# Kernel tuning notes

Hardware: AMD Instinct MI355X
Metric: run time of the kernel (lower is better)

The kernel has to match this reference:

```python
import jax, jax.numpy as jnp
import numpy as np

THRESHOLD = 0.5
ALPHA = 1.0
RATIO = 1.0
BACKGROUND = 0
OBJECT = 1


def cxcywh_to_xyxy(b):
    cxcy, wh = b[..., :2], b[..., 2:]
    return jnp.concatenate([cxcy - wh / 2.0, cxcy + wh / 2.0], axis=-1)


def xyxy_to_cxcywh(b):
    xy1, xy2 = b[..., :2], b[..., 2:]
    return jnp.concatenate([(xy1 + xy2) / 2.0, xy2 - xy1], axis=-1)


def cxcywh_to_gcxgcy(c, d):
    # standard SSD encoding with variances (0.1, 0.2)
    g_cxcy = (c[..., :2] - d[..., :2]) / (d[..., 2:] / 10.0)
    g_wh = jnp.log(c[..., 2:] / d[..., 2:]) * 5.0
    return jnp.concatenate([g_cxcy, g_wh], axis=-1)


def box_iou(a, b):
    # a: [M,4] xyxy, b: [A,4] xyxy -> [M,A]
    area_a = (a[:, 2] - a[:, 0]) * (a[:, 3] - a[:, 1])
    area_b = (b[:, 2] - b[:, 0]) * (b[:, 3] - b[:, 1])
    lt = jnp.maximum(a[:, None, :2], b[None, :, :2])
    rb = jnp.minimum(a[:, None, 2:], b[None, :, 2:])
    wh = jnp.clip(rb - lt, 0.0)
    inter = wh[..., 0] * wh[..., 1]
    return inter / (area_a[:, None] + area_b[None, :] - inter)


def setup_inputs() -> dict:
    B, A, M = 32, 16384, 64
    key = jax.random.key(0)
    k1, k2, k3, k4 = jax.random.split(key, 4)
    x = jax.random.normal(k1, (B, A, 4), dtype=jnp.float32)
    y = jax.random.normal(k2, (B, A, 2), dtype=jnp.float32)
    # valid xyxy GT boxes in [0,1]
    u = jax.random.uniform(k3, (B, M, 4), dtype=jnp.float32)
    xy1 = u[..., :2] * 0.7
    wh = 0.05 + u[..., 2:] * 0.25
    boxes = jnp.concatenate([xy1, xy1 + wh], axis=-1)
    # default (prior) boxes in cxcywh
    ud = jax.random.uniform(k4, (A, 4), dtype=jnp.float32)
    dcxcy = 0.05 + ud[..., :2] * 0.9
    dwh = 0.05 + ud[..., 2:] * 0.25
    default = jnp.concatenate([dcxcy, dwh], axis=-1)
    labels = jnp.ones((B, M), dtype=jnp.int32)  # all GT boxes are 'object'
    return {"x": x, "y": y, "boxes": boxes, "labels": labels, "default": default}


def reference(x, y, boxes, labels, default):
    B, A = x.shape[0], default.shape[0]
    M = boxes.shape[1]
    default_xy = cxcywh_to_xyxy(default)  # [A,4]

    def match(bx):  # bx: [M,4]
        iou = box_iou(bx, default_xy)              # [M,A]
        overlap = iou.max(axis=0)                  # [A] best GT per anchor
        digit = jnp.argmax(iou, axis=0)            # [A]
        best_anchor = jnp.argmax(iou, axis=1)      # [M] best anchor per GT
        digit = digit.at[best_anchor].set(jnp.arange(M))
        overlap = overlap.at[best_anchor].set(1.0)
        return digit, overlap

    digit, overlap = jax.vmap(match)(boxes)        # [B,A], [B,A]
    matched = jnp.take_along_axis(boxes, digit[..., None], axis=1)  # [B,A,4]
    localization = cxcywh_to_gcxgcy(xyxy_to_cxcywh(matched), default)  # [B,A,4]

    gathered = jnp.take_along_axis(labels, digit, axis=1)           # [B,A]
    classification = jnp.where(overlap < THRESHOLD, BACKGROUND, gathered)

    positives = classification == OBJECT
    total = positives.sum()
    totf = total.astype(x.dtype)

    # SmoothL1 (beta=1), mean over positive elements (P*4)
    d = x - localization
    ad = jnp.abs(d)
    sl1 = jnp.where(ad < 1.0, 0.5 * d * d, ad - 0.5)
    smooth = (sl1 * positives[..., None]).sum() / (totf * 4.0)

    # per-anchor cross entropy
    logp = jax.nn.log_softmax(y, axis=-1)                 # [B,A,2]
    ent = -jnp.take_along_axis(logp, classification[..., None], axis=-1)[..., 0]

    pos_sum = jnp.where(positives, ent, 0.0).sum()
    # hard negative mining: sort negatives descending, keep int(total*ratio)
    negv = jnp.where(positives, 0.0, ent).ravel()         # CE >= 0, so masking with 0 is safe
    neg_sorted = jnp.sort(negv)[::-1]
    keep = (totf * RATIO).astype(jnp.int32)
    neg_sum = jnp.where(jnp.arange(negv.shape[0]) < keep, neg_sorted, 0.0).sum()

    entropy = ALPHA * (pos_sum + neg_sum) / totf
    return smooth + entropy
```

## Files before the change

### kernel.cpp

```cpp
#include <hip/hip_runtime.h>

#define THRESH 0.5f

__global__ void __launch_bounds__(256) k_matchboth(
        const float* __restrict__ boxes, const float* __restrict__ dflt,
        unsigned* __restrict__ match, unsigned long long* __restrict__ bestchunk,
        unsigned* __restrict__ zerop, int B, int A, int M, int chunks) {
    __shared__ float4 bx[128];
    __shared__ float barea[128];
    __shared__ float4 anch[256];
    __shared__ float adarea[256];
    __shared__ unsigned long long lm[128];
    int tid = threadIdx.x;
    if (blockIdx.x == 0) {
        for (int j = tid; j < 6160; j += 256) zerop[j] = 0u;
    }
    int b = blockIdx.x / chunks;
    int chunk = blockIdx.x - b * chunks;
    int a = chunk * 256 + tid;
    if (tid < M) {
        float4 bv = *reinterpret_cast<const float4*>(boxes + ((size_t)b * M + tid) * 4);
        bx[tid] = bv;
        barea[tid] = (bv.z - bv.x) * (bv.w - bv.y);
        lm[tid] = 0ull;
    }
    bool aval = (a < A);
    float dx1 = 0.f, dy1 = 0.f, dx2 = 0.f, dy2 = 0.f, darea = 0.f;
    if (aval) {
        float4 dv = *reinterpret_cast<const float4*>(dflt + (size_t)a * 4);
        dx1 = dv.x - dv.z * 0.5f; dy1 = dv.y - dv.w * 0.5f;
        dx2 = dv.x + dv.z * 0.5f; dy2 = dv.y + dv.w * 0.5f;
        darea = (dx2 - dx1) * (dy2 - dy1);
    }
    anch[tid] = make_float4(dx1, dy1, dx2, dy2);
    adarea[tid] = darea;
    __syncthreads();
    if (aval) {
        float binter = -1.0f, bS = 1.0f; int bm = 0;
        #pragma unroll 4
        for (int m = 0; m < M; ++m) {
            float4 bb = bx[m];
            float lx = fmaxf(bb.x, dx1), ly = fmaxf(bb.y, dy1);
            float rx = fminf(bb.z, dx2), ry = fminf(bb.w, dy2);
            float w = fmaxf(rx - lx, 0.f), h = fmaxf(ry - ly, 0.f);
            float inter = w * h;
            float S = barea[m] + darea;
            bool gt = inter * bS > binter * S;
            binter = gt ? inter : binter;
            bS     = gt ? S : bS;
            bm     = gt ? m : bm;
        }
        unsigned fl = (3.0f * binter >= bS) ? (1u << 30) : 0u;
        match[(size_t)b * A + a] = (unsigned)bm | fl;
    }
    int wv = tid >> 6, lane = tid & 63;
    int abase = chunk * 256 + wv * 64;
    int kmax = min(64, A - abase);
    if (lane < M && kmax > 0) {
        float4 bb = bx[lane];
        float ba = barea[lane];
        float binter = -1.0f, bS = 1.0f; int bk = 0;
        #pragma unroll 4
        for (int k = 0; k < kmax; ++k) {
            float4 av = anch[wv * 64 + k];
            float lx = fmaxf(bb.x, av.x), ly = fmaxf(bb.y, av.y);
            float rx = fminf(bb.z, av.z), ry = fminf(bb.w, av.w);
            float w = fmaxf(rx - lx, 0.f), h = fmaxf(ry - ly, 0.f);
            float inter = w * h;
            float S = ba + adarea[wv * 64 + k];
            bool gt = inter * bS > binter * S;
            binter = gt ? inter : binter;
            bS     = gt ? S : bS;
            bk     = gt ? k : bk;
        }
        float best = binter / (bS - binter);
        atomicMax(&lm[lane], ((unsigned long long)__float_as_uint(best) << 32) |
                             (unsigned long long)(unsigned)(~(abase + bk)));
    }
    __syncthreads();
    if (tid < M)
        bestchunk[((size_t)b * chunks + chunk) * M + tid] = lm[tid];
}

__global__ void k_override(const unsigned long long* __restrict__ bestchunk,
                           unsigned* __restrict__ match, int B, int A, int M, int chunks) {
    int i = blockIdx.x * blockDim.x + threadIdx.x;
    if (i >= B * M) return;
    int b = i / M, m = i - b * M;
    const unsigned long long* bp = bestchunk + (size_t)b * chunks * M + m;
    unsigned long long p = 0ull;
    for (int c = 0; c < chunks; ++c) {
        unsigned long long q = bp[(size_t)c * M];
        p = (q > p) ? q : p;
    }
    unsigned a = ~(unsigned)(p & 0xFFFFFFFFull);
    if (a < (unsigned)A)
        atomicMax(&match[(size_t)b * A + a], 0x80000000u | (unsigned)m);
}

__global__ void __launch_bounds__(256) k_main(
        const float* __restrict__ x, const float* __restrict__ y,
        const float* __restrict__ boxes, const int* __restrict__ labels,
        const float* __restrict__ dflt, const unsigned* __restrict__ match,
        float* __restrict__ negv, unsigned* __restrict__ hist1,
        unsigned* __restrict__ scal, int A, int M, int N) {
    __shared__ unsigned lh[2048];
    __shared__ float4 sbx[128];
    __shared__ int slab[128];
    int tid = threadIdx.x;
    int i0 = (blockIdx.x * 256 + tid) * 4;
    int b = (int)(((long long)blockIdx.x * 1024) / A);
    uint4 w4 = *reinterpret_cast<const uint4*>(match + i0);
    const float4* yp = reinterpret_cast<const float4*>(y + (size_t)i0 * 2);
    float4 ya = yp[0], yb = yp[1];
    for (int j = tid; j < 2048; j += 256) lh[j] = 0u;
    if (tid < M) {
        sbx[tid] = *reinterpret_cast<const float4*>(boxes + ((size_t)b * M + tid) * 4);
        slab[tid] = labels[b * M + tid];
    }
    __syncthreads();
    float l_smooth = 0.f, l_pos = 0.f; int l_cnt = 0;
    {
        unsigned wws[4] = {w4.x, w4.y, w4.z, w4.w};
        float y0s[4] = {ya.x, ya.z, yb.x, yb.z};
        float y1s[4] = {ya.y, ya.w, yb.y, yb.w};
        float vs[4];
        int a0 = i0 - b * A;
        #pragma unroll
        for (int e = 0; e < 4; ++e) {
            unsigned w = wws[e];
            int digit = (int)(w & 0xFFFFu);
            bool flag = (w & 0xC0000000u) != 0u;
            int c = flag ? slab[digit] : 0;
            bool pos = (c == 1);
            float y0 = y0s[e], y1v = y1s[e];
            float mx = fmaxf(y0, y1v);
            float lse = mx + log1pf(expf(-fabsf(y0 - y1v)));
            float ent = lse - ((c == 0) ? y0 : y1v);
            float v = pos ? 0.f : ent;
            vs[e] = v;
            if (pos) {
                float4 bv = sbx[digit];
                float4 dv = *reinterpret_cast<const float4*>(dflt + (size_t)(a0 + e) * 4);
                float4 xv = *reinterpret_cast<const float4*>(x + (size_t)(i0 + e) * 4);
                float cw = bv.z - bv.x, ch = bv.w - bv.y;
                float ccx = (bv.x + bv.z) * 0.5f, ccy = (bv.y + bv.w) * 0.5f;
                float l0 = (ccx - dv.x) / (dv.z * 0.1f);
                float l1 = (ccy - dv.y) / (dv.w * 0.1f);
                float l2 = logf(cw / dv.z) * 5.f;
                float l3 = logf(ch / dv.w) * 5.f;
                float s = 0.f, d, ad;
                d = xv.x - l0; ad = fabsf(d); s += (ad < 1.f) ? 0.5f * d * d : ad - 0.5f;
                d = xv.y - l1; ad = fabsf(d); s += (ad < 1.f) ? 0.5f * d * d : ad - 0.5f;
                d = xv.z - l2; ad = fabsf(d); s += (ad < 1.f) ? 0.5f * d * d : ad - 0.5f;
                d = xv.w - l3; ad = fabsf(d); s += (ad < 1.f) ? 0.5f * d * d : ad - 0.5f;
                l_smooth += s; l_pos += ent; l_cnt += 1;
            }
            atomicAdd(&lh[__float_as_uint(v) >> 21], 1u);
        }
        *reinterpret_cast<float4*>(negv + i0) = make_float4(vs[0], vs[1], vs[2], vs[3]);
    }
    for (int off = 32; off > 0; off >>= 1) {
        l_smooth += __shfl_down(l_smooth, off, 64);
        l_pos    += __shfl_down(l_pos, off, 64);
        l_cnt    += __shfl_down(l_cnt, off, 64);
    }
    __shared__ float rs[4], rp[4]; __shared__ int rc[4];
    int wv = tid >> 6;
    if ((tid & 63) == 0) { rs[wv] = l_smooth; rp[wv] = l_pos; rc[wv] = l_cnt; }
    __syncthreads();
    if (tid == 0) {
        float ss = rs[0] + rs[1] + rs[2] + rs[3];
        float pp = rp[0] + rp[1] + rp[2] + rp[3];
        int   cc = rc[0] + rc[1] + rc[2] + rc[3];
        if (ss != 0.f) atomicAdd((float*)&scal[2], ss);
        if (pp != 0.f) atomicAdd((float*)&scal[1], pp);
        if (cc)        atomicAdd((int*)&scal[0], cc);
    }
    __syncthreads();
    for (int j = tid; j < 2048; j += 256) {
        unsigned h = lh[j];
        if (h) atomicAdd(&hist1[j], h);
    }
}

__device__ __forceinline__ void scan_find(const unsigned* hist, int nbins,
                                          unsigned k, unsigned* ts, unsigned* res) {
    int t = threadIdx.x;
    int per = nbins >> 8;
    unsigned s = 0;
    for (int j = 0; j < per; ++j) s += hist[t * per + j];
    ts[t] = s;
    __syncthreads();
    for (int off = 1; off < 256; off <<= 1) {
        unsigned add = (t >= off) ? ts[t - off] : 0u;
        __syncthreads();
        ts[t] += add;
        __syncthreads();
    }
    unsigned total = ts[255];
    unsigned P = (t == 0) ? 0u : ts[t - 1];
    for (int j = 0; j < per; ++j) {
        unsigned h = hist[t * per + j];
        P += h;
        unsigned above = total - P;
        if (above < k && k <= above + h) { res[0] = (unsigned)(t * per + j); res[1] = k - above; }
    }
    __syncthreads();
}

__global__ void __launch_bounds__(256) k_refine2(
        const float* __restrict__ negv, int N, unsigned* __restrict__ scal,
        const unsigned* __restrict__ hist1, unsigned* __restrict__ hist2,
        float* __restrict__ fsum2, float* __restrict__ out) {
    __shared__ unsigned ts[256], res[2];
    __shared__ unsigned lh[2048];
    __shared__ float lf[2048];
    int tid = threadIdx.x;
    scan_find(hist1, 2048, scal[0], ts, res);
    unsigned bin1 = res[0], k1 = res[1];
    for (int j = tid; j < 2048; j += 256) { lh[j] = 0u; lf[j] = 0.f; }
    __syncthreads();
    float sacc = 0.f;
    int i = (blockIdx.x * 256 + tid) * 4;
    if (i + 3 < N) {
        float4 v4 = *reinterpret_cast<const float4*>(negv + i);
        float vv[4] = {v4.x, v4.y, v4.z, v4.w};
        #pragma unroll
        for (int e = 0; e < 4; ++e) {
            unsigned u = __float_as_uint(vv[e]);
            unsigned b1 = u >> 21;
            if (b1 > bin1) sacc += vv[e];
            else if (b1 == bin1) {
                unsigned j = (u >> 10) & 0x7FFu;
                atomicAdd(&lh[j], 1u);
                atomicAdd(&lf[j], vv[e]);
            }
        }
    }
    __syncthreads();
    for (int j = tid; j < 2048; j += 256) {
        unsigned h = lh[j];
        if (h) { atomicAdd(&hist2[j], h); atomicAdd(&fsum2[j], lf[j]); }
    }
    for (int off = 32; off > 0; off >>= 1) sacc += __shfl_down(sacc, off, 64);
    __shared__ float rsum[4];
    __shared__ unsigned isLast;
    int wv = tid >> 6;
    if ((tid & 63) == 0) rsum[wv] = sacc;
    __syncthreads();
    if (tid == 0) {
        float ss = rsum[0] + rsum[1] + rsum[2] + rsum[3];
        if (ss != 0.f) atomicAdd((float*)&scal[9], ss);
        __threadfence();
        unsigned prev = atomicAdd(&scal[12], 1u);
        isLast = (prev == gridDim.x - 1) ? 1u : 0u;
    }
    __syncthreads();
    if (!isLast) return;
    for (int j = tid; j < 2048; j += 256) {
        lh[j] = ((volatile unsigned*)hist2)[j];
        lf[j] = ((volatile float*)fsum2)[j];
    }
    __syncthreads();
    scan_find(lh, 2048, k1, ts, res);
    unsigned bin2 = res[0], k2 = res[1];
    float fs = 0.f;
    for (int j = tid; j < 2048; j += 256)
        if (j > (int)bin2) fs += lf[j];
    for (int off = 32; off > 0; off >>= 1) fs += __shfl_down(fs, off, 64);
    if ((tid & 63) == 0) rsum[wv] = fs;
    __syncthreads();
    if (tid == 0) {
        float fst = rsum[0] + rsum[1] + rsum[2] + rsum[3];
        volatile unsigned* vs = scal;
        volatile float* vf = (volatile float*)scal;
        float k = (float)vs[0];
        float tmid = __uint_as_float((bin1 << 21) | (bin2 << 10) | 512u);
        float neg_sum = vf[9] + fst + (float)k2 * tmid;
        float smooth = vf[2] / (k * 4.f);
        float ent = (vf[1] + neg_sum) / k;
        out[0] = smooth + ent;
    }
}

extern "C" void kernel_launch(void* const* d_in, const int* in_sizes, int n_in,
                              void* d_out, int out_size, void* d_ws, size_t ws_size,
                              hipStream_t stream) {
    const float* x      = (const float*)d_in[0];
    const float* y      = (const float*)d_in[1];
    const float* boxes  = (const float*)d_in[2];
    const int*   labels = (const int*)d_in[3];
    const float* dflt   = (const float*)d_in[4];
    float* out = (float*)d_out;

    int A = in_sizes[4] / 4;
    int B = in_sizes[1] / (2 * A);
    int M = in_sizes[3] / B;
    int N = B * A;
    int chunks = (A + 255) / 256;

    unsigned* ws    = (unsigned*)d_ws;
    unsigned* match = ws;
    float*    negv  = (float*)(ws + (size_t)N);
    unsigned long long* bestchunk = (unsigned long long*)(ws + (size_t)2 * N);
    unsigned* hist1 = ws + (size_t)2 * N + (size_t)2 * B * chunks * M;
    unsigned* hist2 = hist1 + 2048;
    float*    fsum2 = (float*)(hist2 + 2048);
    unsigned* scal  = (unsigned*)(fsum2 + 2048);

    k_matchboth<<<dim3(B * chunks), dim3(256), 0, stream>>>(boxes, dflt, match, bestchunk,
                                                            hist1, B, A, M, chunks);
    k_override<<<dim3((B * M + 255) / 256), dim3(256), 0, stream>>>(bestchunk, match, B, A, M, chunks);
    k_main<<<dim3(N / 1024), dim3(256), 0, stream>>>(x, y, boxes, labels, dflt, match,
                                                     negv, hist1, scal, A, M, N);
    k_refine2<<<dim3(N / 1024), dim3(256), 0, stream>>>(negv, N, scal, hist1, hist2, fsum2, out);
}
```

Measured before the change: 161.7 us.

## Reduce per-box best anchor with global atomics and load x/default unconditionally

The per-chunk best-anchor array and the loop over chunks in k_override are replaced by a 64-bit atomicMax into one slot per (batch, box). A separate zeroing kernel now clears that slot array and the histogram and scalar buffers. In k_main, the x and default-box rows are loaded as contiguous vector loads up front and the SmoothL1 terms are computed for every anchor, which avoids divergent scattered loads at the cost of extra log/divide work. An extra kernel launch is added and the N bounds check in k_refine2 is dropped.

```diff
diff --git a/kernel.cpp b/kernel.cpp
--- a/kernel.cpp
+++ b/kernel.cpp
@@ -1,20 +1,22 @@
 #include <hip/hip_runtime.h>
 
 #define THRESH 0.5f
+
+__global__ void k_zero(unsigned* __restrict__ p, int n) {
+    int i = blockIdx.x * blockDim.x + threadIdx.x;
+    if (i < n) p[i] = 0u;
+}
 
 __global__ void __launch_bounds__(256) k_matchboth(
         const float* __restrict__ boxes, const float* __restrict__ dflt,
-        unsigned* __restrict__ match, unsigned long long* __restrict__ bestchunk,
-        unsigned* __restrict__ zerop, int B, int A, int M, int chunks) {
+        unsigned* __restrict__ match, unsigned long long* __restrict__ bestbox,
+        int B, int A, int M, int chunks) {
     __shared__ float4 bx[128];
     __shared__ float barea[128];
     __shared__ float4 anch[256];
     __shared__ float adarea[256];
     __shared__ unsigned long long lm[128];
     int tid = threadIdx.x;
-    if (blockIdx.x == 0) {
-        for (int j = tid; j < 6160; j += 256) zerop[j] = 0u;
-    }
     int b = blockIdx.x / chunks;
     int chunk = blockIdx.x - b * chunks;
     int a = chunk * 256 + tid;
@@ -78,24 +80,22 @@
                              (unsigned long long)(unsigned)(~(abase + bk)));
     }
     __syncthreads();
-    if (tid < M)
-        bestchunk[((size_t)b * chunks + chunk) * M + tid] = lm[tid];
-}
-
-__global__ void k_override(const unsigned long long* __restrict__ bestchunk,
-                           unsigned* __restrict__ match, int B, int A, int M, int chunks) {
+    if (tid < M) {
+        unsigned long long p = lm[tid];
+        if (p) atomicMax(&bestbox[(size_t)b * M + tid], p);
+    }
+}
+
+__global__ void k_override(const unsigned long long* __restrict__ bestbox,
+                           unsigned* __restrict__ match, int B, int A, int M) {
     int i = blockIdx.x * blockDim.x + threadIdx.x;
     if (i >= B * M) return;
-    int b = i / M, m = i - b * M;
-    const unsigned long long* bp = bestchunk + (size_t)b * chunks * M + m;
-    unsigned long long p = 0ull;
-    for (int c = 0; c < chunks; ++c) {
-        unsigned long long q = bp[(size_t)c * M];
-        p = (q > p) ? q : p;
-    }
+    unsigned long long p = bestbox[i];
     unsigned a = ~(unsigned)(p & 0xFFFFFFFFull);
-    if (a < (unsigned)A)
+    if (a < (unsigned)A) {
+        int b = i / M, m = i % M;
         atomicMax(&match[(size_t)b * A + a], 0x80000000u | (unsigned)m);
+    }
 }
 
 __global__ void __launch_bounds__(256) k_main(
@@ -110,9 +110,14 @@
     int tid = threadIdx.x;
     int i0 = (blockIdx.x * 256 + tid) * 4;
     int b = (int)(((long long)blockIdx.x * 1024) / A);
+    int a0 = i0 - b * A;
     uint4 w4 = *reinterpret_cast<const uint4*>(match + i0);
     const float4* yp = reinterpret_cast<const float4*>(y + (size_t)i0 * 2);
     float4 ya = yp[0], yb = yp[1];
+    const float4* xp = reinterpret_cast<const float4*>(x + (size_t)i0 * 4);
+    float4 xs[4] = {xp[0], xp[1], xp[2], xp[3]};
+    const float4* dp = reinterpret_cast<const float4*>(dflt + (size_t)a0 * 4);
+    float4 ds[4] = {dp[0], dp[1], dp[2], dp[3]};
     for (int j = tid; j < 2048; j += 256) lh[j] = 0u;
     if (tid < M) {
         sbx[tid] = *reinterpret_cast<const float4*>(boxes + ((size_t)b * M + tid) * 4);
@@ -125,7 +130,6 @@
         float y0s[4] = {ya.x, ya.z, yb.x, yb.z};
         float y1s[4] = {ya.y, ya.w, yb.y, yb.w};
         float vs[4];
-        int a0 = i0 - b * A;
         #pragma unroll
         for (int e = 0; e < 4; ++e) {
             unsigned w = wws[e];
@@ -133,29 +137,27 @@
             bool flag = (w & 0xC0000000u) != 0u;
             int c = flag ? slab[digit] : 0;
             bool pos = (c == 1);
+            float4 bv = sbx[digit];
+            float4 dv = ds[e];
+            float cw = bv.z - bv.x, ch = bv.w - bv.y;
+            float ccx = (bv.x + bv.z) * 0.5f, ccy = (bv.y + bv.w) * 0.5f;
+            float l0 = (ccx - dv.x) / (dv.z * 0.1f);
+            float l1 = (ccy - dv.y) / (dv.w * 0.1f);
+            float l2 = logf(cw / dv.z) * 5.f;
+            float l3 = logf(ch / dv.w) * 5.f;
+            float4 xv = xs[e];
+            float s = 0.f, d, ad;
+            d = xv.x - l0; ad = fabsf(d); s += (ad < 1.f) ? 0.5f * d * d : ad - 0.5f;
+            d = xv.y - l1; ad = fabsf(d); s += (ad < 1.f) ? 0.5f * d * d : ad - 0.5f;
+            d = xv.z - l2; ad = fabsf(d); s += (ad < 1.f) ? 0.5f * d * d : ad - 0.5f;
+            d = xv.w - l3; ad = fabsf(d); s += (ad < 1.f) ? 0.5f * d * d : ad - 0.5f;
             float y0 = y0s[e], y1v = y1s[e];
             float mx = fmaxf(y0, y1v);
             float lse = mx + log1pf(expf(-fabsf(y0 - y1v)));
             float ent = lse - ((c == 0) ? y0 : y1v);
             float v = pos ? 0.f : ent;
             vs[e] = v;
-            if (pos) {
-                float4 bv = sbx[digit];
-                float4 dv = *reinterpret_cast<const float4*>(dflt + (size_t)(a0 + e) * 4);
-                float4 xv = *reinterpret_cast<const float4*>(x + (size_t)(i0 + e) * 4);
-                float cw = bv.z - bv.x, ch = bv.w - bv.y;
-                float ccx = (bv.x + bv.z) * 0.5f, ccy = (bv.y + bv.w) * 0.5f;
-                float l0 = (ccx - dv.x) / (dv.z * 0.1f);
-                float l1 = (ccy - dv.y) / (dv.w * 0.1f);
-                float l2 = logf(cw / dv.z) * 5.f;
-                float l3 = logf(ch / dv.w) * 5.f;
-                float s = 0.f, d, ad;
-                d = xv.x - l0; ad = fabsf(d); s += (ad < 1.f) ? 0.5f * d * d : ad - 0.5f;
-                d = xv.y - l1; ad = fabsf(d); s += (ad < 1.f) ? 0.5f * d * d : ad - 0.5f;
-                d = xv.z - l2; ad = fabsf(d); s += (ad < 1.f) ? 0.5f * d * d : ad - 0.5f;
-                d = xv.w - l3; ad = fabsf(d); s += (ad < 1.f) ? 0.5f * d * d : ad - 0.5f;
-                l_smooth += s; l_pos += ent; l_cnt += 1;
-            }
+            if (pos) { l_smooth += s; l_pos += ent; l_cnt += 1; }
             atomicAdd(&lh[__float_as_uint(v) >> 21], 1u);
         }
         *reinterpret_cast<float4*>(negv + i0) = make_float4(vs[0], vs[1], vs[2], vs[3]);
@@ -223,7 +225,7 @@
     __syncthreads();
     float sacc = 0.f;
     int i = (blockIdx.x * 256 + tid) * 4;
-    if (i + 3 < N) {
+    {
         float4 v4 = *reinterpret_cast<const float4*>(negv + i);
         float vv[4] = {v4.x, v4.y, v4.z, v4.w};
         #pragma unroll
@@ -303,15 +305,16 @@
     unsigned* ws    = (unsigned*)d_ws;
     unsigned* match = ws;
     float*    negv  = (float*)(ws + (size_t)N);
-    unsigned long long* bestchunk = (unsigned long long*)(ws + (size_t)2 * N);
-    unsigned* hist1 = ws + (size_t)2 * N + (size_t)2 * B * chunks * M;
+    unsigned long long* bestbox = (unsigned long long*)(ws + (size_t)2 * N);
+    unsigned* hist1 = ws + (size_t)2 * N + 2 * B * M;
     unsigned* hist2 = hist1 + 2048;
     float*    fsum2 = (float*)(hist2 + 2048);
     unsigned* scal  = (unsigned*)(fsum2 + 2048);
-
-    k_matchboth<<<dim3(B * chunks), dim3(256), 0, stream>>>(boxes, dflt, match, bestchunk,
-                                                            hist1, B, A, M, chunks);
-    k_override<<<dim3((B * M + 255) / 256), dim3(256), 0, stream>>>(bestchunk, match, B, A, M, chunks);
+    int nzero = 2 * B * M + 2048 * 3 + 16;
+
+    k_zero<<<dim3((nzero + 255) / 256), dim3(256), 0, stream>>>(ws + (size_t)2 * N, nzero);
+    k_matchboth<<<dim3(B * chunks), dim3(256), 0, stream>>>(boxes, dflt, match, bestbox, B, A, M, chunks);
+    k_override<<<dim3((B * M + 255) / 256), dim3(256), 0, stream>>>(bestbox, match, B, A, M);
     k_main<<<dim3(N / 1024), dim3(256), 0, stream>>>(x, y, boxes, labels, dflt, match,
                                                      negv, hist1, scal, A, M, N);
     k_refine2<<<dim3(N / 1024), dim3(256), 0, stream>>>(negv, N, scal, hist1, hist2, fsum2, out);
```

Result: faster. 146.9 us (-9.2%).
